# Kernel tuning notes

Measured on AMD Instinct MI355X. Metric: run time of the kernel, lower is better.

Reference implementation:

```python
import jax, jax.numpy as jnp
import numpy as np

B, T, C, HD = 4, 4096, 1024, 64  # batch, seq, n_embd, head_dim = n_embd//n_head


def setup_inputs() -> dict:
    key = jax.random.key(0)
    k1, k2, k3, k4 = jax.random.split(key, 4)
    scale = 0.02
    return {
        "x": jax.random.normal(k1, (B, T, C), dtype=jnp.float32),
        "Wq": jax.random.normal(k2, (C, HD), dtype=jnp.float32) * scale,
        "Wk": jax.random.normal(k3, (C, HD), dtype=jnp.float32) * scale,
        "Wv": jax.random.normal(k4, (C, HD), dtype=jnp.float32) * scale,
    }


def reference(x, Wq, Wk, Wv):
    # single-head projections: [B,T,C] @ [C,HD] -> [B,T,HD]
    q = jnp.einsum("btc,ch->bth", x, Wq)
    k = jnp.einsum("btc,ch->bth", x, Wk)
    v = jnp.einsum("btc,ch->bth", x, Wv)
    scale = k.shape[-1] ** -0.5
    # scores: [B,T,T], causal mask via -inf, stable softmax
    alpha = jnp.einsum("bqh,bkh->bqk", q, k) * scale
    t = x.shape[1]
    causal = jnp.tril(jnp.ones((t, t), dtype=bool))
    alpha = jnp.where(causal, alpha, -jnp.inf)
    alpha = jax.nn.softmax(alpha, axis=-1)
    # dropout p=0.0 -> identity
    h = jnp.einsum("bqk,bkh->bqh", alpha, v)
    return h
```

## Files before the change

kernel.cpp:

```cpp
#include <hip/hip_runtime.h>

#define T_SEQ 4096
#define C_DIM 1024
#define HD 64

typedef __attribute__((ext_vector_type(8))) __bf16 bf16x8;
typedef __attribute__((ext_vector_type(8))) unsigned short us8;
typedef __attribute__((ext_vector_type(4))) unsigned short us4;
typedef __attribute__((ext_vector_type(4))) float f32x4;

#define QSCALE 0.18033688011112042f

__device__ __forceinline__ unsigned short f2bf(float f) {
    union { float f; unsigned u; } x; x.f = f;
    unsigned r = x.u + 0x7FFFu + ((x.u >> 16) & 1u);
    return (unsigned short)(r >> 16);
}

__device__ __forceinline__ us8 cvt8(float4 a, float4 b) {
    union { __bf16 h[8]; us8 v; } u;
    u.h[0] = (__bf16)a.x; u.h[1] = (__bf16)a.y; u.h[2] = (__bf16)a.z; u.h[3] = (__bf16)a.w;
    u.h[4] = (__bf16)b.x; u.h[5] = (__bf16)b.y; u.h[6] = (__bf16)b.z; u.h[7] = (__bf16)b.w;
    return u.v;
}

__global__ __launch_bounds__(256) void k_wtrans(const float* __restrict__ Wq,
                                                const float* __restrict__ Wk,
                                                const float* __restrict__ Wv,
                                                unsigned short* __restrict__ wt_g) {
    __shared__ unsigned short tile[64][72];
    const int bx = blockIdx.x;
    const int which = bx >> 4;
    const int k0 = (bx & 15) * 64;
    const float* W = (which == 0) ? Wq : ((which == 1) ? Wk : Wv);
    const int t = threadIdx.x;
    {
        const int r = t >> 2, c0 = (t & 3) * 16;
        const float4* src = reinterpret_cast<const float4*>(W + (k0 + r) * HD + c0);
        #pragma unroll
        for (int i = 0; i < 4; ++i) {
            float4 v = src[i];
            tile[r][c0 + 4 * i + 0] = f2bf(v.x);
            tile[r][c0 + 4 * i + 1] = f2bf(v.y);
            tile[r][c0 + 4 * i + 2] = f2bf(v.z);
            tile[r][c0 + 4 * i + 3] = f2bf(v.w);
        }
    }
    __syncthreads();
    {
        const int n = t >> 2, kc0 = (t & 3) * 16;
        alignas(16) unsigned short o[16];
        #pragma unroll
        for (int i = 0; i < 16; ++i) o[i] = tile[kc0 + i][n];
        unsigned short* dst = wt_g + (size_t)(which * 64 + n) * 1024 + k0 + kc0;
        *reinterpret_cast<us8*>(dst)     = *reinterpret_cast<const us8*>(&o[0]);
        *reinterpret_cast<us8*>(dst + 8) = *reinterpret_cast<const us8*>(&o[8]);
    }
}

__global__ __launch_bounds__(256) void k_proj(const float* __restrict__ x,
                                              const unsigned short* __restrict__ wt_g,
                                              unsigned short* __restrict__ qs,
                                              unsigned short* __restrict__ ksb,
                                              unsigned short* __restrict__ vt) {
    __shared__ unsigned short smem[6656];
    unsigned short* xs0 = smem;
    unsigned short* xs1 = smem + 2304;
    const int tid = threadIdx.x;
    const int w = tid >> 6, lane = tid & 63;
    const int l15 = lane & 15, g = lane >> 4;
    const int m0 = blockIdx.x * 32;
    const int sr = tid >> 3, sc0 = (tid & 7) * 8;
    const float* xrow = x + (size_t)(m0 + sr) * C_DIM + sc0;
    const unsigned short* wrow[3];
    #pragma unroll
    for (int mf = 0; mf < 3; ++mf)
        wrow[mf] = wt_g + (size_t)((3 * w + mf) * 16 + l15) * C_DIM + g * 8;

    f32x4 acc[3][2];
    #pragma unroll
    for (int mf = 0; mf < 3; ++mf)
        #pragma unroll
        for (int nf = 0; nf < 2; ++nf)
            acc[mf][nf] = (f32x4){0.f, 0.f, 0.f, 0.f};

    {
        float4 xa = *reinterpret_cast<const float4*>(xrow);
        float4 xb = *reinterpret_cast<const float4*>(xrow + 4);
        *reinterpret_cast<us8*>(xs0 + sr * 72 + sc0) = cvt8(xa, xb);
    }
    us8 wc[3][2];
    #pragma unroll
    for (int mf = 0; mf < 3; ++mf)
        #pragma unroll
        for (int k2 = 0; k2 < 2; ++k2)
            wc[mf][k2] = *reinterpret_cast<const us8*>(wrow[mf] + k2 * 32);
    __syncthreads();

    for (int kk = 0; kk < 16; ++kk) {
        unsigned short* xcur = (kk & 1) ? xs1 : xs0;
        unsigned short* xnxt = (kk & 1) ? xs0 : xs1;
        const bool pf = (kk < 15);
        float4 na, nb;
        us8 wn[3][2];
        if (pf) {
            na = *reinterpret_cast<const float4*>(xrow + (kk + 1) * 64);
            nb = *reinterpret_cast<const float4*>(xrow + (kk + 1) * 64 + 4);
            #pragma unroll
            for (int mf = 0; mf < 3; ++mf)
                #pragma unroll
                for (int k2 = 0; k2 < 2; ++k2)
                    wn[mf][k2] = *reinterpret_cast<const us8*>(wrow[mf] + (kk + 1) * 64 + k2 * 32);
        }
        #pragma unroll
        for (int k2 = 0; k2 < 2; ++k2) {
            bf16x8 bfr[2];
            #pragma unroll
            for (int nf = 0; nf < 2; ++nf)
                bfr[nf] = *reinterpret_cast<const bf16x8*>(xcur + (nf * 16 + l15) * 72 + k2 * 32 + g * 8);
            #pragma unroll
            for (int mf = 0; mf < 3; ++mf) {
                bf16x8 afr = *reinterpret_cast<const bf16x8*>(&wc[mf][k2]);
                #pragma unroll
                for (int nf = 0; nf < 2; ++nf)
                    acc[mf][nf] = __builtin_amdgcn_mfma_f32_16x16x32_bf16(
                        afr, bfr[nf], acc[mf][nf], 0, 0, 0);
            }
        }
        if (pf) {
            *reinterpret_cast<us8*>(xnxt + sr * 72 + sc0) = cvt8(na, nb);
            #pragma unroll
            for (int mf = 0; mf < 3; ++mf)
                #pragma unroll
                for (int k2 = 0; k2 < 2; ++k2)
                    wc[mf][k2] = wn[mf][k2];
        }
        __syncthreads();
    }

    unsigned short* out_lds = smem;
    #pragma unroll
    for (int mf = 0; mf < 3; ++mf) {
        const int Mfr = 3 * w + mf;
        const float s = (Mfr < 4) ? QSCALE : 1.0f;
        #pragma unroll
        for (int nf = 0; nf < 2; ++nf) {
            union { __bf16 h[4]; us4 v; } u;
            #pragma unroll
            for (int r = 0; r < 4; ++r) u.h[r] = (__bf16)(acc[mf][nf][r] * s);
            *reinterpret_cast<us4*>(out_lds + (nf * 16 + l15) * 208 + Mfr * 16 + 4 * g) = u.v;
        }
    }
    __syncthreads();
    {
        const int r = tid >> 3, c = (tid & 7) * 8;
        const size_t gm = (size_t)(m0 + r);
        *reinterpret_cast<us8*>(qs + gm * 64 + c)  = *reinterpret_cast<const us8*>(out_lds + r * 208 + c);
        *reinterpret_cast<us8*>(ksb + gm * 64 + c) = *reinterpret_cast<const us8*>(out_lds + r * 208 + 64 + c);
    }
    {
        const int d = tid >> 2, j0 = (tid & 3) * 8;
        const int b = m0 >> 12, t0 = m0 & 4095;
        alignas(16) unsigned short tmp[8];
        #pragma unroll
        for (int j = 0; j < 8; ++j) tmp[j] = out_lds[(j0 + j) * 208 + 128 + d];
        *reinterpret_cast<us8*>(vt + (size_t)(b * 64 + d) * T_SEQ + t0 + j0) =
            *reinterpret_cast<const us8*>(tmp);
    }
}

__global__ __launch_bounds__(256) void k_attn(const unsigned short* __restrict__ qs,
                                              const unsigned short* __restrict__ ks,
                                              const unsigned short* __restrict__ vt,
                                              float* __restrict__ Opart,
                                              float* __restrict__ mlw) {
    __shared__ unsigned short kbuf[2][64 * 72];
    __shared__ unsigned short vbuf[2][64 * 72];
    __shared__ unsigned short p_lds[4][16 * 72];
    const int tid = threadIdx.x;
    const int w = tid >> 6, lane = tid & 63;
    const int l15 = lane & 15, g = lane >> 4;
    const int batch = blockIdx.y;
    const int i = blockIdx.x;
    const int a = (i < 16) ? 0 : (i < 48) ? 1 : (i < 96) ? 2 : 3;
    const int rem = i - 8 * a * (a + 1);
    const int b = rem / (a + 1);
    const int s = rem - b * (a + 1);
    const int qt = 16 * a + b;
    const int it0 = s * 16;
    const int it1 = min(it0 + 16, qt + 1);
    const int q0 = qt * 64;
    const int qi = q0 + 16 * w + l15;
    const size_t qrow = (size_t)batch * T_SEQ + qi;

    bf16x8 qfrag[2];
    qfrag[0] = *reinterpret_cast<const bf16x8*>(qs + qrow * 64 + g * 8);
    qfrag[1] = *reinterpret_cast<const bf16x8*>(qs + qrow * 64 + 32 + g * 8);

    f32x4 accO[4];
    #pragma unroll
    for (int df = 0; df < 4; ++df) accO[df] = (f32x4){0.f, 0.f, 0.f, 0.f};
    float m_run = -1e30f, l_run = 0.f;

    const int sr = tid >> 2, sc0 = (tid & 3) * 16;
    const unsigned short* kbase = ks + ((size_t)batch * T_SEQ + sr) * 64 + sc0;
    const unsigned short* vbase = vt + ((size_t)batch * 64 + sr) * T_SEQ + sc0;

    {
        us8 a0 = *reinterpret_cast<const us8*>(kbase + (size_t)it0 * 4096);
        us8 a1 = *reinterpret_cast<const us8*>(kbase + (size_t)it0 * 4096 + 8);
        us8 b0 = *reinterpret_cast<const us8*>(vbase + it0 * 64);
        us8 b1 = *reinterpret_cast<const us8*>(vbase + it0 * 64 + 8);
        unsigned short* kd = &kbuf[0][0] + sr * 72 + sc0;
        unsigned short* vd = &vbuf[0][0] + sr * 72 + sc0;
        *reinterpret_cast<us8*>(kd) = a0; *reinterpret_cast<us8*>(kd + 8) = a1;
        *reinterpret_cast<us8*>(vd) = b0; *reinterpret_cast<us8*>(vd + 8) = b1;
    }
    __syncthreads();

    for (int it = it0; it < it1; ++it) {
        const int cur = (it - it0) & 1;
        const bool pf = (it + 1 < it1);
        us8 n0, n1, n2, n3;
        if (pf) {
            n0 = *reinterpret_cast<const us8*>(kbase + (size_t)(it + 1) * 4096);
            n1 = *reinterpret_cast<const us8*>(kbase + (size_t)(it + 1) * 4096 + 8);
            n2 = *reinterpret_cast<const us8*>(vbase + (it + 1) * 64);
            n3 = *reinterpret_cast<const us8*>(vbase + (it + 1) * 64 + 8);
        }
        const unsigned short* kt  = &kbuf[cur][0];
        const unsigned short* vti = &vbuf[cur][0];
        f32x4 sfr[4];
        #pragma unroll
        for (int kf = 0; kf < 4; ++kf) sfr[kf] = (f32x4){0.f, 0.f, 0.f, 0.f};
        #pragma unroll
        for (int k2 = 0; k2 < 2; ++k2) {
            #pragma unroll
            for (int kf = 0; kf < 4; ++kf) {
                bf16x8 afr = *reinterpret_cast<const bf16x8*>(kt + (kf * 16 + l15) * 72 + k2 * 32 + g * 8);
                sfr[kf] = __builtin_amdgcn_mfma_f32_16x16x32_bf16(afr, qfrag[k2], sfr[kf], 0, 0, 0);
            }
        }
        if (it == qt) {
            #pragma unroll
            for (int kf = 0; kf < 4; ++kf) {
                #pragma unroll
                for (int r = 0; r < 4; ++r) {
                    const int kidx = it * 64 + kf * 16 + 4 * g + r;
                    if (kidx > qi) sfr[kf][r] = -1e30f;
                }
            }
        }
        float mx = -1e30f;
        #pragma unroll
        for (int kf = 0; kf < 4; ++kf)
            #pragma unroll
            for (int r = 0; r < 4; ++r) mx = fmaxf(mx, sfr[kf][r]);
        mx = fmaxf(mx, __shfl_xor(mx, 16, 64));
        mx = fmaxf(mx, __shfl_xor(mx, 32, 64));
        if (!__all(mx <= m_run)) {
            const float m_new = fmaxf(m_run, mx);
            const float alpha = exp2f(m_run - m_new);
            l_run *= alpha;
            #pragma unroll
            for (int df = 0; df < 4; ++df) accO[df] *= alpha;
            m_run = m_new;
        }
        float psum = 0.f;
        unsigned short* pw = &p_lds[w][0];
        #pragma unroll
        for (int kf = 0; kf < 4; ++kf) {
            union { __bf16 h[4]; us4 v; } up;
            #pragma unroll
            for (int r = 0; r < 4; ++r) {
                const float p = exp2f(sfr[kf][r] - m_run);
                psum += p;
                up.h[r] = (__bf16)p;
            }
            *reinterpret_cast<us4*>(pw + l15 * 72 + kf * 16 + 4 * g) = up.v;
        }
        psum += __shfl_xor(psum, 16, 64);
        psum += __shfl_xor(psum, 32, 64);
        l_run += psum;
        bf16x8 bp0 = *reinterpret_cast<const bf16x8*>(pw + l15 * 72 + g * 8);
        bf16x8 bp1 = *reinterpret_cast<const bf16x8*>(pw + l15 * 72 + 32 + g * 8);
        #pragma unroll
        for (int df = 0; df < 4; ++df) {
            bf16x8 a0 = *reinterpret_cast<const bf16x8*>(vti + (df * 16 + l15) * 72 + g * 8);
            bf16x8 a1 = *reinterpret_cast<const bf16x8*>(vti + (df * 16 + l15) * 72 + 32 + g * 8);
            accO[df] = __builtin_amdgcn_mfma_f32_16x16x32_bf16(a0, bp0, accO[df], 0, 0, 0);
            accO[df] = __builtin_amdgcn_mfma_f32_16x16x32_bf16(a1, bp1, accO[df], 0, 0, 0);
        }
        if (pf) {
            unsigned short* kd = &kbuf[cur ^ 1][0] + sr * 72 + sc0;
            unsigned short* vd = &vbuf[cur ^ 1][0] + sr * 72 + sc0;
            *reinterpret_cast<us8*>(kd) = n0; *reinterpret_cast<us8*>(kd + 8) = n1;
            *reinterpret_cast<us8*>(vd) = n2; *reinterpret_cast<us8*>(vd + 8) = n3;
        }
        __syncthreads();
    }

    const int pb = batch * 160 + i;
    float* ob = Opart + (size_t)pb * 4096 + (16 * w + l15) * 64;
    #pragma unroll
    for (int df = 0; df < 4; ++df)
        *reinterpret_cast<f32x4*>(ob + 16 * df + 4 * g) = accO[df];
    if (g == 0) {
        float* mlp = mlw + (size_t)pb * 128 + (16 * w + l15) * 2;
        mlp[0] = m_run;
        mlp[1] = l_run;
    }
}

__global__ __launch_bounds__(256) void k_combine(const float* __restrict__ Opart,
                                                 const float* __restrict__ mlw,
                                                 float* __restrict__ out) {
    const int qt = blockIdx.x, batch = blockIdx.y;
    const int t = threadIdx.x;
    const int r = t >> 2, c = (t & 3) * 16;
    const int a = qt >> 4, b = qt & 15;
    const int nsp = a + 1;
    const int pb0 = batch * 160 + 8 * a * (a + 1) + (a + 1) * b;
    float m_g = -1e30f;
    for (int s = 0; s < nsp; ++s)
        m_g = fmaxf(m_g, mlw[(size_t)(pb0 + s) * 128 + r * 2]);
    float den = 0.f;
    f32x4 num[4];
    #pragma unroll
    for (int j = 0; j < 4; ++j) num[j] = (f32x4){0.f, 0.f, 0.f, 0.f};
    for (int s = 0; s < nsp; ++s) {
        const float* mlp = mlw + (size_t)(pb0 + s) * 128 + r * 2;
        const float wgt = exp2f(mlp[0] - m_g);
        den += wgt * mlp[1];
        const f32x4* op = reinterpret_cast<const f32x4*>(
            Opart + (size_t)(pb0 + s) * 4096 + r * 64 + c);
        #pragma unroll
        for (int j = 0; j < 4; ++j) num[j] += op[j] * wgt;
    }
    const float inv = 1.f / den;
    f32x4* o = reinterpret_cast<f32x4*>(out + ((size_t)batch * T_SEQ + qt * 64 + r) * 64 + c);
    #pragma unroll
    for (int j = 0; j < 4; ++j) o[j] = num[j] * inv;
}

extern "C" void kernel_launch(void* const* d_in, const int* in_sizes, int n_in,
                              void* d_out, int out_size, void* d_ws, size_t ws_size,
                              hipStream_t stream) {
    (void)in_sizes; (void)n_in; (void)out_size; (void)ws_size;
    const float* x  = (const float*)d_in[0];
    const float* Wq = (const float*)d_in[1];
    const float* Wk = (const float*)d_in[2];
    const float* Wv = (const float*)d_in[3];
    float* out = (float*)d_out;
    unsigned short* ws16 = (unsigned short*)d_ws;
    unsigned short* wt_g = ws16;
    unsigned short* qsb  = ws16 + 196608;
    unsigned short* ksb  = qsb + 1048576;
    unsigned short* vtb  = ksb + 1048576;
    float* Opart = (float*)(vtb + 1048576);
    float* mlw   = Opart + 640 * 4096;
    k_wtrans <<<dim3(48),      dim3(256), 0, stream>>>(Wq, Wk, Wv, wt_g);
    k_proj   <<<dim3(512),     dim3(256), 0, stream>>>(x, wt_g, qsb, ksb, vtb);
    k_attn   <<<dim3(160, 4),  dim3(256), 0, stream>>>(qsb, ksb, vtb, Opart, mlw);
    k_combine<<<dim3(64, 4),   dim3(256), 0, stream>>>(Opart, mlw, out);
}
```

Baseline: 74.65 us.

## Refine attention split-K granularity, swizzle LDS, store partials in bf16, skip combine for unsplit tiles

The attention split-K chunk drops from 16 to 8 key tiles, giving 288 blocks per batch launched heaviest-first to improve load balance on the causal triangle. Tiles that need only one split now normalize and write the output directly, and the combine kernel handles only the remaining 56 tiles. Partial outputs are stored as bf16 to halve combine traffic, at some precision cost. LDS padding is replaced by an XOR swizzle in one shared buffer, and s_setprio is raised around the MFMA sections.

```diff
diff --git a/kernel.cpp b/kernel.cpp
--- a/kernel.cpp
+++ b/kernel.cpp
@@ -15,6 +15,11 @@
     union { float f; unsigned u; } x; x.f = f;
     unsigned r = x.u + 0x7FFFu + ((x.u >> 16) & 1u);
     return (unsigned short)(r >> 16);
+}
+
+__device__ __forceinline__ float bf2f(unsigned short u) {
+    union { unsigned u; float f; } x; x.u = ((unsigned)u) << 16;
+    return x.f;
 }
 
 __device__ __forceinline__ us8 cvt8(float4 a, float4 b) {
@@ -22,6 +27,10 @@
     u.h[0] = (__bf16)a.x; u.h[1] = (__bf16)a.y; u.h[2] = (__bf16)a.z; u.h[3] = (__bf16)a.w;
     u.h[4] = (__bf16)b.x; u.h[5] = (__bf16)b.y; u.h[6] = (__bf16)b.z; u.h[7] = (__bf16)b.w;
     return u.v;
+}
+
+__device__ __forceinline__ int swzs(int idx) {
+    return idx ^ ((((idx) >> 6) & 7) << 3);
 }
 
 __global__ __launch_bounds__(256) void k_wtrans(const float* __restrict__ Wq,
@@ -172,25 +181,25 @@
 __global__ __launch_bounds__(256) void k_attn(const unsigned short* __restrict__ qs,
                                               const unsigned short* __restrict__ ks,
                                               const unsigned short* __restrict__ vt,
-                                              float* __restrict__ Opart,
-                                              float* __restrict__ mlw) {
-    __shared__ unsigned short kbuf[2][64 * 72];
-    __shared__ unsigned short vbuf[2][64 * 72];
-    __shared__ unsigned short p_lds[4][16 * 72];
+                                              unsigned short* __restrict__ Opart,
+                                              float* __restrict__ mlw,
+                                              float* __restrict__ out) {
+    __shared__ unsigned short sm[20480];
     const int tid = threadIdx.x;
     const int w = tid >> 6, lane = tid & 63;
     const int l15 = lane & 15, g = lane >> 4;
     const int batch = blockIdx.y;
-    const int i = blockIdx.x;
-    const int a = (i < 16) ? 0 : (i < 48) ? 1 : (i < 96) ? 2 : 3;
-    const int rem = i - 8 * a * (a + 1);
+    const int i = 287 - blockIdx.x;
+    const int a = (i < 8) ? 0 : (i < 24) ? 1 : (i < 48) ? 2 : (i < 80) ? 3 :
+                  (i < 120) ? 4 : (i < 168) ? 5 : (i < 224) ? 6 : 7;
+    const int rem = i - 4 * a * (a + 1);
     const int b = rem / (a + 1);
     const int s = rem - b * (a + 1);
-    const int qt = 16 * a + b;
-    const int it0 = s * 16;
-    const int it1 = min(it0 + 16, qt + 1);
-    const int q0 = qt * 64;
-    const int qi = q0 + 16 * w + l15;
+    const int qt = 8 * a + b;
+    const int ns = a + 1;
+    const int it0 = s * 8;
+    const int it1 = min(it0 + 8, qt + 1);
+    const int qi = qt * 64 + 16 * w + l15;
     const size_t qrow = (size_t)batch * T_SEQ + qi;
 
     bf16x8 qfrag[2];
@@ -205,16 +214,18 @@
     const int sr = tid >> 2, sc0 = (tid & 3) * 16;
     const unsigned short* kbase = ks + ((size_t)batch * T_SEQ + sr) * 64 + sc0;
     const unsigned short* vbase = vt + ((size_t)batch * 64 + sr) * T_SEQ + sc0;
+    const int pbase = 16384 + w * 1024;
 
     {
         us8 a0 = *reinterpret_cast<const us8*>(kbase + (size_t)it0 * 4096);
         us8 a1 = *reinterpret_cast<const us8*>(kbase + (size_t)it0 * 4096 + 8);
         us8 b0 = *reinterpret_cast<const us8*>(vbase + it0 * 64);
         us8 b1 = *reinterpret_cast<const us8*>(vbase + it0 * 64 + 8);
-        unsigned short* kd = &kbuf[0][0] + sr * 72 + sc0;
-        unsigned short* vd = &vbuf[0][0] + sr * 72 + sc0;
-        *reinterpret_cast<us8*>(kd) = a0; *reinterpret_cast<us8*>(kd + 8) = a1;
-        *reinterpret_cast<us8*>(vd) = b0; *reinterpret_cast<us8*>(vd + 8) = b1;
+        const int kd = sr * 64 + sc0, vd = 8192 + sr * 64 + sc0;
+        *reinterpret_cast<us8*>(sm + swzs(kd))     = a0;
+        *reinterpret_cast<us8*>(sm + swzs(kd + 8)) = a1;
+        *reinterpret_cast<us8*>(sm + swzs(vd))     = b0;
+        *reinterpret_cast<us8*>(sm + swzs(vd + 8)) = b1;
     }
     __syncthreads();
 
@@ -228,19 +239,22 @@
             n2 = *reinterpret_cast<const us8*>(vbase + (it + 1) * 64);
             n3 = *reinterpret_cast<const us8*>(vbase + (it + 1) * 64 + 8);
         }
-        const unsigned short* kt  = &kbuf[cur][0];
-        const unsigned short* vti = &vbuf[cur][0];
+        const int kb = cur * 4096;
+        const int vb = 8192 + cur * 4096;
         f32x4 sfr[4];
         #pragma unroll
         for (int kf = 0; kf < 4; ++kf) sfr[kf] = (f32x4){0.f, 0.f, 0.f, 0.f};
+        __builtin_amdgcn_s_setprio(1);
         #pragma unroll
         for (int k2 = 0; k2 < 2; ++k2) {
             #pragma unroll
             for (int kf = 0; kf < 4; ++kf) {
-                bf16x8 afr = *reinterpret_cast<const bf16x8*>(kt + (kf * 16 + l15) * 72 + k2 * 32 + g * 8);
+                bf16x8 afr = *reinterpret_cast<const bf16x8*>(
+                    sm + swzs(kb + (kf * 16 + l15) * 64 + k2 * 32 + g * 8));
                 sfr[kf] = __builtin_amdgcn_mfma_f32_16x16x32_bf16(afr, qfrag[k2], sfr[kf], 0, 0, 0);
             }
         }
+        __builtin_amdgcn_s_setprio(0);
         if (it == qt) {
             #pragma unroll
             for (int kf = 0; kf < 4; ++kf) {
@@ -251,11 +265,11 @@
                 }
             }
         }
-        float mx = -1e30f;
-        #pragma unroll
-        for (int kf = 0; kf < 4; ++kf)
-            #pragma unroll
-            for (int r = 0; r < 4; ++r) mx = fmaxf(mx, sfr[kf][r]);
+        float m0 = fmaxf(fmaxf(sfr[0][0], sfr[0][1]), fmaxf(sfr[0][2], sfr[0][3]));
+        float m1 = fmaxf(fmaxf(sfr[1][0], sfr[1][1]), fmaxf(sfr[1][2], sfr[1][3]));
+        float m2 = fmaxf(fmaxf(sfr[2][0], sfr[2][1]), fmaxf(sfr[2][2], sfr[2][3]));
+        float m3 = fmaxf(fmaxf(sfr[3][0], sfr[3][1]), fmaxf(sfr[3][2], sfr[3][3]));
+        float mx = fmaxf(fmaxf(m0, m1), fmaxf(m2, m3));
         mx = fmaxf(mx, __shfl_xor(mx, 16, 64));
         mx = fmaxf(mx, __shfl_xor(mx, 32, 64));
         if (!__all(mx <= m_run)) {
@@ -267,7 +281,6 @@
             m_run = m_new;
         }
         float psum = 0.f;
-        unsigned short* pw = &p_lds[w][0];
         #pragma unroll
         for (int kf = 0; kf < 4; ++kf) {
             union { __bf16 h[4]; us4 v; } up;
@@ -277,50 +290,69 @@
                 psum += p;
                 up.h[r] = (__bf16)p;
             }
-            *reinterpret_cast<us4*>(pw + l15 * 72 + kf * 16 + 4 * g) = up.v;
+            *reinterpret_cast<us4*>(sm + swzs(pbase + l15 * 64 + kf * 16 + 4 * g)) = up.v;
         }
         psum += __shfl_xor(psum, 16, 64);
         psum += __shfl_xor(psum, 32, 64);
         l_run += psum;
-        bf16x8 bp0 = *reinterpret_cast<const bf16x8*>(pw + l15 * 72 + g * 8);
-        bf16x8 bp1 = *reinterpret_cast<const bf16x8*>(pw + l15 * 72 + 32 + g * 8);
+        bf16x8 bp0 = *reinterpret_cast<const bf16x8*>(sm + swzs(pbase + l15 * 64 + g * 8));
+        bf16x8 bp1 = *reinterpret_cast<const bf16x8*>(sm + swzs(pbase + l15 * 64 + 32 + g * 8));
+        __builtin_amdgcn_s_setprio(1);
         #pragma unroll
         for (int df = 0; df < 4; ++df) {
-            bf16x8 a0 = *reinterpret_cast<const bf16x8*>(vti + (df * 16 + l15) * 72 + g * 8);
-            bf16x8 a1 = *reinterpret_cast<const bf16x8*>(vti + (df * 16 + l15) * 72 + 32 + g * 8);
+            bf16x8 a0 = *reinterpret_cast<const bf16x8*>(
+                sm + swzs(vb + (df * 16 + l15) * 64 + g * 8));
+            bf16x8 a1 = *reinterpret_cast<const bf16x8*>(
+                sm + swzs(vb + (df * 16 + l15) * 64 + 32 + g * 8));
             accO[df] = __builtin_amdgcn_mfma_f32_16x16x32_bf16(a0, bp0, accO[df], 0, 0, 0);
             accO[df] = __builtin_amdgcn_mfma_f32_16x16x32_bf16(a1, bp1, accO[df], 0, 0, 0);
         }
+        __builtin_amdgcn_s_setprio(0);
         if (pf) {
-            unsigned short* kd = &kbuf[cur ^ 1][0] + sr * 72 + sc0;
-            unsigned short* vd = &vbuf[cur ^ 1][0] + sr * 72 + sc0;
-            *reinterpret_cast<us8*>(kd) = n0; *reinterpret_cast<us8*>(kd + 8) = n1;
-            *reinterpret_cast<us8*>(vd) = n2; *reinterpret_cast<us8*>(vd + 8) = n3;
+            const int kd = (cur ^ 1) * 4096 + sr * 64 + sc0;
+            const int vd = 8192 + (cur ^ 1) * 4096 + sr * 64 + sc0;
+            *reinterpret_cast<us8*>(sm + swzs(kd))     = n0;
+            *reinterpret_cast<us8*>(sm + swzs(kd + 8)) = n1;
+            *reinterpret_cast<us8*>(sm + swzs(vd))     = n2;
+            *reinterpret_cast<us8*>(sm + swzs(vd + 8)) = n3;
         }
         __syncthreads();
     }
 
-    const int pb = batch * 160 + i;
-    float* ob = Opart + (size_t)pb * 4096 + (16 * w + l15) * 64;
-    #pragma unroll
-    for (int df = 0; df < 4; ++df)
-        *reinterpret_cast<f32x4*>(ob + 16 * df + 4 * g) = accO[df];
-    if (g == 0) {
-        float* mlp = mlw + (size_t)pb * 128 + (16 * w + l15) * 2;
-        mlp[0] = m_run;
-        mlp[1] = l_run;
-    }
-}
-
-__global__ __launch_bounds__(256) void k_combine(const float* __restrict__ Opart,
+    if (ns == 1) {
+        const float inv = 1.0f / l_run;
+        #pragma unroll
+        for (int df = 0; df < 4; ++df) {
+            f32x4 o = accO[df] * inv;
+            *reinterpret_cast<f32x4*>(out + qrow * 64 + df * 16 + 4 * g) = o;
+        }
+    } else {
+        const int pb = batch * 288 + i;
+        unsigned short* ob = Opart + (size_t)pb * 4096 + (16 * w + l15) * 64;
+        #pragma unroll
+        for (int df = 0; df < 4; ++df) {
+            union { __bf16 h[4]; us4 v; } u;
+            #pragma unroll
+            for (int r = 0; r < 4; ++r) u.h[r] = (__bf16)accO[df][r];
+            *reinterpret_cast<us4*>(ob + 16 * df + 4 * g) = u.v;
+        }
+        if (g == 0) {
+            float* mlp = mlw + (size_t)pb * 128 + (16 * w + l15) * 2;
+            mlp[0] = m_run;
+            mlp[1] = l_run;
+        }
+    }
+}
+
+__global__ __launch_bounds__(256) void k_combine(const unsigned short* __restrict__ Opart,
                                                  const float* __restrict__ mlw,
                                                  float* __restrict__ out) {
-    const int qt = blockIdx.x, batch = blockIdx.y;
+    const int qt = 8 + blockIdx.x, batch = blockIdx.y;
     const int t = threadIdx.x;
     const int r = t >> 2, c = (t & 3) * 16;
-    const int a = qt >> 4, b = qt & 15;
+    const int a = qt >> 3;
     const int nsp = a + 1;
-    const int pb0 = batch * 160 + 8 * a * (a + 1) + (a + 1) * b;
+    const int pb0 = batch * 288 + 4 * a * (a + 1) + (qt & 7) * (a + 1);
     float m_g = -1e30f;
     for (int s = 0; s < nsp; ++s)
         m_g = fmaxf(m_g, mlw[(size_t)(pb0 + s) * 128 + r * 2]);
@@ -332,10 +364,14 @@
         const float* mlp = mlw + (size_t)(pb0 + s) * 128 + r * 2;
         const float wgt = exp2f(mlp[0] - m_g);
         den += wgt * mlp[1];
-        const f32x4* op = reinterpret_cast<const f32x4*>(
-            Opart + (size_t)(pb0 + s) * 4096 + r * 64 + c);
-        #pragma unroll
-        for (int j = 0; j < 4; ++j) num[j] += op[j] * wgt;
+        const unsigned short* op = Opart + (size_t)(pb0 + s) * 4096 + r * 64 + c;
+        us8 v0 = *reinterpret_cast<const us8*>(op);
+        us8 v1 = *reinterpret_cast<const us8*>(op + 8);
+        #pragma unroll
+        for (int j = 0; j < 8; ++j) {
+            num[j >> 2][j & 3] += wgt * bf2f(v0[j]);
+            num[2 + (j >> 2)][j & 3] += wgt * bf2f(v1[j]);
+        }
     }
     const float inv = 1.f / den;
     f32x4* o = reinterpret_cast<f32x4*>(out + ((size_t)batch * T_SEQ + qt * 64 + r) * 64 + c);
@@ -357,10 +393,10 @@
     unsigned short* qsb  = ws16 + 196608;
     unsigned short* ksb  = qsb + 1048576;
     unsigned short* vtb  = ksb + 1048576;
-    float* Opart = (float*)(vtb + 1048576);
-    float* mlw   = Opart + 640 * 4096;
+    unsigned short* Opart = vtb + 1048576;
+    float* mlw = (float*)(Opart + 4718592);
     k_wtrans <<<dim3(48),      dim3(256), 0, stream>>>(Wq, Wk, Wv, wt_g);
     k_proj   <<<dim3(512),     dim3(256), 0, stream>>>(x, wt_g, qsb, ksb, vtb);
-    k_attn   <<<dim3(160, 4),  dim3(256), 0, stream>>>(qsb, ksb, vtb, Opart, mlw);
-    k_combine<<<dim3(64, 4),   dim3(256), 0, stream>>>(Opart, mlw, out);
-}
+    k_attn   <<<dim3(288, 4),  dim3(256), 0, stream>>>(qsb, ksb, vtb, Opart, mlw, out);
+    k_combine<<<dim3(56, 4),   dim3(256), 0, stream>>>(Opart, mlw, out);
+}
```

New measurement: 73.71 us. Within noise of the previous version (-1.3%).
